# Kernel optimization log

Measured on AMD Instinct MI355X. Metric: run time of the kernel, lower is better.

Reference implementation:

```python
import jax, jax.numpy as jnp
import numpy as np

N_NODE = 4096
N_FEA_IN = 128
N_FEA_OUT = 128


def setup_inputs() -> dict:
    key = jax.random.key(0)
    k_x, k_a, k_w, k_att = jax.random.split(key, 4)
    stdv_w = 1.0 / np.sqrt(N_FEA_OUT)       # torch reset: 1/sqrt(W.size(1))
    stdv_a = 1.0 / np.sqrt(2 * N_FEA_OUT)   # a is [1, 2*n_fea_out]
    X = jax.random.normal(k_x, (N_NODE, N_FEA_IN), dtype=jnp.float32)
    A = jax.random.uniform(k_a, (N_NODE, N_NODE), dtype=jnp.float32)  # dense weighted adjacency
    W = jax.random.uniform(k_w, (N_FEA_IN, N_FEA_OUT), minval=-stdv_w, maxval=stdv_w, dtype=jnp.float32)
    a = jax.random.uniform(k_att, (1, 2 * N_FEA_OUT), minval=-stdv_a, maxval=stdv_a, dtype=jnp.float32)
    return {"X": X, "A": A, "W": W, "a": a}


def reference(X, A, W, a):
    # XW: [N, F_out]
    XW = jnp.matmul(X, W)
    f = W.shape[1]
    # Z[i,j] = concat(XW[j], XW[i]); Z @ a.T decomposes into two rank-1 broadcasts:
    s_col = jnp.matmul(XW, a[0, :f])   # depends on column index j
    s_row = jnp.matmul(XW, a[0, f:])   # depends on row index i
    Z1 = jax.nn.leaky_relu(s_row[:, None] + s_col[None, :], negative_slope=0.01)  # [N, N]
    den = jnp.exp(Z1)                  # [N, N]
    num = jnp.matmul(A, den)           # numerator[i,j] = sum_k A[i,k] * den[k,j]
    # vectorized replacement of the Python double loop: att = den/num where num != 0
    att = jnp.where(num != 0, den / jnp.where(num != 0, num, 1.0), 0.0)
    H = jnp.matmul(A, jnp.matmul(att, XW))
    return H
```

## Files before the change

kernel.cpp:

```cpp
#include <hip/hip_runtime.h>
#include <hip/hip_bf16.h>
#include <stdint.h>

#define NN 4096
#define NF 128
#define NSPLIT 16
#define XROWS 4

using f32x4  = __attribute__((ext_vector_type(4))) float;
using bf16x8 = __attribute__((ext_vector_type(8))) __bf16;
using u16x8  = __attribute__((ext_vector_type(8))) uint16_t;

__device__ __forceinline__ uint16_t f2b(float f) {
    union { float f; uint32_t u; } v; v.f = f;
    uint32_t r = v.u + 0x7FFFu + ((v.u >> 16) & 1u);
    return (uint16_t)(r >> 16);
}

__device__ __forceinline__ float b2f(uint16_t u) {
    union { uint32_t u; float f; } v; v.u = ((uint32_t)u) << 16;
    return v.f;
}

__global__ __launch_bounds__(128) void xw_kernel(
    const float* __restrict__ X, const float* __restrict__ W,
    const float* __restrict__ a,
    uint16_t* __restrict__ XWT,
    float* __restrict__ s_col, float* __restrict__ s_row) {
    __shared__ float xs[XROWS][NF];
    __shared__ float red[XROWS][2][2];
    const int i0 = blockIdx.x * XROWS, f = threadIdx.x;
    #pragma unroll
    for (int r = 0; r < XROWS; ++r) xs[r][f] = X[(size_t)(i0 + r) * NF + f];
    __syncthreads();
    float acc[XROWS] = {0.f, 0.f, 0.f, 0.f};
    #pragma unroll 4
    for (int k = 0; k < NF; ++k) {
        const float w = W[k * NF + f];
        #pragma unroll
        for (int r = 0; r < XROWS; ++r) acc[r] += xs[r][k] * w;
    }
    ushort4 xo;
    xo.x = f2b(acc[0]); xo.y = f2b(acc[1]); xo.z = f2b(acc[2]); xo.w = f2b(acc[3]);
    *(ushort4*)(XWT + (size_t)f * NN + i0) = xo;
    const float a1 = a[f], a2 = a[NF + f];
    #pragma unroll
    for (int r = 0; r < XROWS; ++r) {
        float sc = acc[r] * a1;
        float sr = acc[r] * a2;
        #pragma unroll
        for (int off = 32; off; off >>= 1) {
            sc += __shfl_down(sc, off);
            sr += __shfl_down(sr, off);
        }
        if ((f & 63) == 0) { red[r][f >> 6][0] = sc; red[r][f >> 6][1] = sr; }
    }
    __syncthreads();
    if (f < XROWS) {
        s_col[i0 + f] = red[f][0][0] + red[f][1][0];
        s_row[i0 + f] = red[f][0][1] + red[f][1][1];
    }
}

__global__ __launch_bounds__(256) void prep_kernel(
    const float* __restrict__ s_row, const float* __restrict__ s_col,
    int* __restrict__ ks, float* __restrict__ w1s, float* __restrict__ w2s,
    float4* __restrict__ rec) {
    __shared__ __align__(16) float sr[NN];
    const int t = threadIdx.x;
    #pragma unroll
    for (int c = 0; c < 16; ++c) sr[t + c * 256] = s_row[t + c * 256];
    __syncthreads();
    const bool isC = blockIdx.x >= 128;
    const int tgt = (blockIdx.x & 127) * 32 + (t >> 3);
    const int sub = t & 7;
    const float4* sr4 = (const float4*)sr;
    int cnt = 0;
    if (!isC) {
        const float s = sr[tgt];
        #pragma unroll 4
        for (int q = 0; q < 128; ++q) {
            const int k4 = q * 8 + sub;
            float4 v = sr4[k4];
            const int kb = k4 * 4;
            cnt += (v.x < s) | ((v.x == s) & (kb + 0 < tgt));
            cnt += (v.y < s) | ((v.y == s) & (kb + 1 < tgt));
            cnt += (v.z < s) | ((v.z == s) & (kb + 2 < tgt));
            cnt += (v.w < s) | ((v.w == s) & (kb + 3 < tgt));
        }
    } else {
        const float th = -s_col[tgt];
        #pragma unroll 4
        for (int q = 0; q < 128; ++q) {
            float4 v = sr4[q * 8 + sub];
            cnt += (v.x <= th) + (v.y <= th) + (v.z <= th) + (v.w <= th);
        }
    }
    cnt += __shfl_down(cnt, 4);
    cnt += __shfl_down(cnt, 2);
    cnt += __shfl_down(cnt, 1);
    if (sub == 0) {
        if (!isC) {
            const float s = sr[tgt];
            ks[cnt]  = tgt;
            w1s[cnt] = __expf(s);
            w2s[cnt] = __expf(0.01f * s);
        } else {
            const float sc = s_col[tgt];
            rec[tgt] = (float4){__int_as_float(cnt), __expf(sc), __expf(0.01f * sc), sc};
        }
    }
}

#define PB(b) ((b) + (((b) >> 4) << 1))

__global__ __launch_bounds__(512, 8) void row_kernel(
    const float* __restrict__ A,
    const float* __restrict__ s_row,
    const int* __restrict__ ks, const float* __restrict__ w1s, const float* __restrict__ w2s,
    const float4* __restrict__ rec,
    uint16_t* __restrict__ Ab, uint16_t* __restrict__ att) {
    __shared__ __align__(16) float rowA[NN];
    __shared__ __align__(16) uint16_t S1[4640];
    __shared__ __align__(16) uint16_t S2[4640];
    __shared__ float wtot[2][8];
    const int i = blockIdx.x, t = threadIdx.x;

    {
        const float4* Ar = (const float4*)(A + (size_t)i * NN);
        ushort4* Abr = (ushort4*)(Ab + (size_t)i * NN);
        #pragma unroll
        for (int c = 0; c < 2; ++c) {
            float4 v = Ar[t + c * 512];
            ((float4*)rowA)[t + c * 512] = v;
            ushort4 o; o.x = f2b(v.x); o.y = f2b(v.y); o.z = f2b(v.z); o.w = f2b(v.w);
            Abr[t + c * 512] = o;
        }
    }
    __syncthreads();

    float l1[8], l2[8];
    {
        const int4*   k4 = (const int4*)ks;
        const float4* a4 = (const float4*)w1s;
        const float4* b4 = (const float4*)w2s;
        float run1 = 0.f, run2 = 0.f;
        #pragma unroll
        for (int g = 0; g < 2; ++g) {
            int4   kk = k4[2 * t + g];
            float4 wa = a4[2 * t + g];
            float4 wb = b4[2 * t + g];
            float g0 = rowA[kk.x], g1 = rowA[kk.y], g2 = rowA[kk.z], g3 = rowA[kk.w];
            run1 += g0 * wa.x; l1[4 * g + 0] = run1;  run2 += g0 * wb.x; l2[4 * g + 0] = run2;
            run1 += g1 * wa.y; l1[4 * g + 1] = run1;  run2 += g1 * wb.y; l2[4 * g + 1] = run2;
            run1 += g2 * wa.z; l1[4 * g + 2] = run1;  run2 += g2 * wb.z; l2[4 * g + 2] = run2;
            run1 += g3 * wa.w; l1[4 * g + 3] = run1;  run2 += g3 * wb.w; l2[4 * g + 3] = run2;
        }
    }
    float s1 = l1[7], s2 = l2[7];
    const int lane = t & 63, wid = t >> 6;
    #pragma unroll
    for (int off = 1; off < 64; off <<= 1) {
        float u1 = __shfl_up(s1, off);
        float u2 = __shfl_up(s2, off);
        if (lane >= off) { s1 += u1; s2 += u2; }
    }
    if (lane == 63) { wtot[0][wid] = s1; wtot[1][wid] = s2; }
    __syncthreads();

    float off1 = 0.f, off2 = 0.f, tot1 = 0.f, tot2 = 0.f;
    #pragma unroll
    for (int w = 0; w < 8; ++w) {
        const float va = wtot[0][w], vb = wtot[1][w];
        tot1 += va; tot2 += vb;
        if (w < wid) { off1 += va; off2 += vb; }
    }
    const float ex1 = off1 + s1 - l1[7];
    const float ex2 = off2 + s2 - l2[7];
    {
        uint32_t* q1 = (uint32_t*)S1;
        uint32_t* q2 = (uint32_t*)S2;
        const int qb = t * 4 + (t >> 1);
        #pragma unroll
        for (int m = 0; m < 4; ++m) {
            const float pl1 = m ? l1[2 * m - 1] : 0.f;
            const float pl2 = m ? l2[2 * m - 1] : 0.f;
            const float sa = tot1 - ex1 - pl1;
            const float sb = tot1 - ex1 - l1[2 * m];
            const float pa = ex2 + pl2;
            const float pb = ex2 + l2[2 * m];
            q1[qb + m] = (uint32_t)f2b(sa) | ((uint32_t)f2b(sb) << 16);
            q2[qb + m] = (uint32_t)f2b(pa) | ((uint32_t)f2b(pb) << 16);
        }
    }
    if (t == 511) {
        S1[PB(4096)] = 0;
        S2[PB(4096)] = f2b(tot2);
    }
    __syncthreads();

    const float sri = s_row[i];
    uint32_t* attR = (uint32_t*)(att + (size_t)i * NN);
    #pragma unroll
    for (int e = 0; e < 4; ++e) {
        const int j0 = e * 1024 + 2 * t;
        const float4 ra = rec[j0];
        const float4 rb = rec[j0 + 1];
        const int Ca = __float_as_int(ra.x);
        const int Cb = __float_as_int(rb.x);
        const float numa = ra.y * b2f(S1[PB(Ca)]) + ra.z * b2f(S2[PB(Ca)]);
        const float numb = rb.y * b2f(S1[PB(Cb)]) + rb.z * b2f(S2[PB(Cb)]);
        float za = sri + ra.w; za = za > 0.f ? za : 0.01f * za;
        float zb = sri + rb.w; zb = zb > 0.f ? zb : 0.01f * zb;
        const float dena = __expf(za);
        const float denb = __expf(zb);
        const float va = (numa != 0.f) ? dena * __builtin_amdgcn_rcpf(numa) : 0.f;
        const float vb = (numb != 0.f) ? denb * __builtin_amdgcn_rcpf(numb) : 0.f;
        attR[e * 512 + t] = (uint32_t)f2b(va) | ((uint32_t)f2b(vb) << 16);
    }
}

__global__ __launch_bounds__(256) void gemm_splitk_kernel(
    const uint16_t* __restrict__ Abt, const uint16_t* __restrict__ Bt,
    float* __restrict__ P) {
    const int bm0 = blockIdx.y * 128;
    const int split = blockIdx.z;
    const int kBeg = split * (NN / NSPLIT);
    const int lane = threadIdx.x & 63, wid = threadIdx.x >> 6;
    const int wy = wid >> 1, wx = wid & 1;
    const int quad = lane >> 4, l16 = lane & 15;

    f32x4 acc[4][4];
    #pragma unroll
    for (int mi = 0; mi < 4; ++mi)
        #pragma unroll
        for (int ni = 0; ni < 4; ++ni)
            acc[mi][ni] = (f32x4){0.f, 0.f, 0.f, 0.f};

    const uint16_t* Ap = Abt + (size_t)(bm0 + wy * 64 + l16) * NN + quad * 8;
    const uint16_t* Bp = Bt  + (size_t)(wx * 64 + l16) * NN + quad * 8;

    #pragma unroll 2
    for (int kk = 0; kk < NN / NSPLIT; kk += 32) {
        const int k0 = kBeg + kk;
        bf16x8 af[4], bf[4];
        #pragma unroll
        for (int mi = 0; mi < 4; ++mi)
            af[mi] = *(const bf16x8*)(Ap + (size_t)(mi * 16) * NN + k0);
        #pragma unroll
        for (int ni = 0; ni < 4; ++ni)
            bf[ni] = *(const bf16x8*)(Bp + (size_t)(ni * 16) * NN + k0);
        #pragma unroll
        for (int mi = 0; mi < 4; ++mi)
            #pragma unroll
            for (int ni = 0; ni < 4; ++ni)
                acc[mi][ni] = __builtin_amdgcn_mfma_f32_16x16x32_bf16(af[mi], bf[ni], acc[mi][ni], 0, 0, 0);
    }

    float* Pp = P + (size_t)split * (NN * NF);
    #pragma unroll
    for (int mi = 0; mi < 4; ++mi) {
        const int i0 = bm0 + wy * 64 + mi * 16 + quad * 4;
        #pragma unroll
        for (int ni = 0; ni < 4; ++ni) {
            const int j = wx * 64 + ni * 16 + l16;
            *(f32x4*)(Pp + (size_t)j * NN + i0) = acc[mi][ni];
        }
    }
}

__global__ __launch_bounds__(256) void reduce_t_kernel(
    const float* __restrict__ P, uint16_t* __restrict__ M1T) {
    const int idx = (blockIdx.x * 256 + threadIdx.x) * 4;
    f32x4 s = (f32x4){0.f, 0.f, 0.f, 0.f};
    #pragma unroll
    for (int sp = 0; sp < NSPLIT; ++sp)
        s += *(const f32x4*)(P + (size_t)sp * (NN * NF) + idx);
    ushort4 o;
    o.x = f2b(s[0]); o.y = f2b(s[1]); o.z = f2b(s[2]); o.w = f2b(s[3]);
    *(ushort4*)(M1T + idx) = o;
}

__global__ __launch_bounds__(256) void reduce_out_kernel(
    const float* __restrict__ P, float* __restrict__ out) {
    __shared__ float acc[NF][17];
    const int i0 = blockIdx.x * 16;
    const int t = threadIdx.x;
    const int ii = t & 15, jb = t >> 4;
    float local[8];
    #pragma unroll
    for (int jj = 0; jj < 8; ++jj) local[jj] = 0.f;
    for (int sp = 0; sp < NSPLIT; ++sp) {
        const float* Pp = P + (size_t)sp * (NN * NF) + i0 + ii;
        #pragma unroll
        for (int jj = 0; jj < 8; ++jj)
            local[jj] += Pp[(size_t)(jb + jj * 16) * NN];
    }
    #pragma unroll
    for (int jj = 0; jj < 8; ++jj) acc[jb + jj * 16][ii] = local[jj];
    __syncthreads();
    const int j = t & 127, rb = t >> 7;
    #pragma unroll
    for (int p = 0; p < 8; ++p) {
        const int r = rb + p * 2;
        out[(size_t)(i0 + r) * NF + j] = acc[j][r];
    }
}

extern "C" void kernel_launch(void* const* d_in, const int* in_sizes, int n_in,
                              void* d_out, int out_size, void* d_ws, size_t ws_size,
                              hipStream_t stream) {
    (void)in_sizes; (void)n_in; (void)out_size; (void)ws_size;
    const float* X = (const float*)d_in[0];
    const float* A = (const float*)d_in[1];
    const float* W = (const float*)d_in[2];
    const float* a = (const float*)d_in[3];
    float* H = (float*)d_out;

    char* ws = (char*)d_ws;
    uint16_t* Ab  = (uint16_t*)(ws);
    uint16_t* att = (uint16_t*)(ws + ((size_t)32 << 20));
    float*    P   = (float*)   (ws + ((size_t)64 << 20));
    uint16_t* XWT = (uint16_t*)(ws + ((size_t)96 << 20));
    uint16_t* M1T = (uint16_t*)(ws + ((size_t)97 << 20));
    char* sm = ws + ((size_t)64 << 20);
    float*  s_col = (float*) (sm);
    float*  s_row = (float*) (sm + (16 << 10));
    int*    ks    = (int*)   (sm + (32 << 10));
    float*  w1s   = (float*) (sm + (48 << 10));
    float*  w2s   = (float*) (sm + (64 << 10));
    float4* rec   = (float4*)(sm + (80 << 10));

    xw_kernel<<<NN / XROWS, NF, 0, stream>>>(X, W, a, XWT, s_col, s_row);
    prep_kernel<<<256, 256, 0, stream>>>(s_row, s_col, ks, w1s, w2s, rec);
    row_kernel<<<NN, 512, 0, stream>>>(A, s_row, ks, w1s, w2s, rec, Ab, att);
    gemm_splitk_kernel<<<dim3(1, 32, NSPLIT), 256, 0, stream>>>(att, XWT, P);
    reduce_t_kernel<<<(NN * NF / 4) / 256, 256, 0, stream>>>(P, M1T);
    gemm_splitk_kernel<<<dim3(1, 32, NSPLIT), 256, 0, stream>>>(Ab, M1T, P);
    reduce_out_kernel<<<NN / 16, 256, 0, stream>>>(P, H);
}
```

Measured before the change: 209.9 us.

## Halve GEMM block tile and software-pipeline split-K register loads

```diff
diff --git a/kernel.cpp b/kernel.cpp
--- a/kernel.cpp
+++ b/kernel.cpp
@@ -220,47 +220,60 @@
     }
 }
 
+#define GLOAD(af, bf, kq)                                                     \
+    {                                                                         \
+        af[0] = *(const bf16x8*)(Ap + (size_t)0  * NN + (kq));                \
+        af[1] = *(const bf16x8*)(Ap + (size_t)16 * NN + (kq));                \
+        bf[0] = *(const bf16x8*)(Bp + (size_t)0  * NN + (kq));                \
+        bf[1] = *(const bf16x8*)(Bp + (size_t)16 * NN + (kq));                \
+        bf[2] = *(const bf16x8*)(Bp + (size_t)32 * NN + (kq));                \
+        bf[3] = *(const bf16x8*)(Bp + (size_t)48 * NN + (kq));                \
+    }
+
+#define MFMA_SET(af, bf)                                                      \
+    {                                                                         \
+        _Pragma("unroll")                                                     \
+        for (int mi = 0; mi < 2; ++mi)                                        \
+            _Pragma("unroll")                                                 \
+            for (int ni = 0; ni < 4; ++ni)                                    \
+                acc[mi][ni] = __builtin_amdgcn_mfma_f32_16x16x32_bf16(        \
+                    af[mi], bf[ni], acc[mi][ni], 0, 0, 0);                    \
+    }
+
 __global__ __launch_bounds__(256) void gemm_splitk_kernel(
     const uint16_t* __restrict__ Abt, const uint16_t* __restrict__ Bt,
     float* __restrict__ P) {
-    const int bm0 = blockIdx.y * 128;
+    const int bm0 = blockIdx.y * 64;
     const int split = blockIdx.z;
     const int kBeg = split * (NN / NSPLIT);
     const int lane = threadIdx.x & 63, wid = threadIdx.x >> 6;
     const int wy = wid >> 1, wx = wid & 1;
     const int quad = lane >> 4, l16 = lane & 15;
 
-    f32x4 acc[4][4];
-    #pragma unroll
-    for (int mi = 0; mi < 4; ++mi)
+    f32x4 acc[2][4];
+    #pragma unroll
+    for (int mi = 0; mi < 2; ++mi)
         #pragma unroll
         for (int ni = 0; ni < 4; ++ni)
             acc[mi][ni] = (f32x4){0.f, 0.f, 0.f, 0.f};
 
-    const uint16_t* Ap = Abt + (size_t)(bm0 + wy * 64 + l16) * NN + quad * 8;
+    const uint16_t* Ap = Abt + (size_t)(bm0 + wy * 32 + l16) * NN + quad * 8;
     const uint16_t* Bp = Bt  + (size_t)(wx * 64 + l16) * NN + quad * 8;
 
-    #pragma unroll 2
-    for (int kk = 0; kk < NN / NSPLIT; kk += 32) {
-        const int k0 = kBeg + kk;
-        bf16x8 af[4], bf[4];
-        #pragma unroll
-        for (int mi = 0; mi < 4; ++mi)
-            af[mi] = *(const bf16x8*)(Ap + (size_t)(mi * 16) * NN + k0);
-        #pragma unroll
-        for (int ni = 0; ni < 4; ++ni)
-            bf[ni] = *(const bf16x8*)(Bp + (size_t)(ni * 16) * NN + k0);
-        #pragma unroll
-        for (int mi = 0; mi < 4; ++mi)
-            #pragma unroll
-            for (int ni = 0; ni < 4; ++ni)
-                acc[mi][ni] = __builtin_amdgcn_mfma_f32_16x16x32_bf16(af[mi], bf[ni], acc[mi][ni], 0, 0, 0);
+    bf16x8 a0[2], b0[4], a1[2], b1[4];
+    GLOAD(a0, b0, kBeg);
+    #pragma unroll
+    for (int kk = 0; kk < NN / NSPLIT; kk += 64) {
+        GLOAD(a1, b1, kBeg + kk + 32);
+        MFMA_SET(a0, b0);
+        if (kk + 64 < NN / NSPLIT) GLOAD(a0, b0, kBeg + kk + 64);
+        MFMA_SET(a1, b1);
     }
 
     float* Pp = P + (size_t)split * (NN * NF);
     #pragma unroll
-    for (int mi = 0; mi < 4; ++mi) {
-        const int i0 = bm0 + wy * 64 + mi * 16 + quad * 4;
+    for (int mi = 0; mi < 2; ++mi) {
+        const int i0 = bm0 + wy * 32 + mi * 16 + quad * 4;
         #pragma unroll
         for (int ni = 0; ni < 4; ++ni) {
             const int j = wx * 64 + ni * 16 + l16;
@@ -334,8 +347,8 @@
     xw_kernel<<<NN / XROWS, NF, 0, stream>>>(X, W, a, XWT, s_col, s_row);
     prep_kernel<<<256, 256, 0, stream>>>(s_row, s_col, ks, w1s, w2s, rec);
     row_kernel<<<NN, 512, 0, stream>>>(A, s_row, ks, w1s, w2s, rec, Ab, att);
-    gemm_splitk_kernel<<<dim3(1, 32, NSPLIT), 256, 0, stream>>>(att, XWT, P);
+    gemm_splitk_kernel<<<dim3(1, 64, NSPLIT), 256, 0, stream>>>(att, XWT, P);
     reduce_t_kernel<<<(NN * NF / 4) / 256, 256, 0, stream>>>(P, M1T);
-    gemm_splitk_kernel<<<dim3(1, 32, NSPLIT), 256, 0, stream>>>(Ab, M1T, P);
+    gemm_splitk_kernel<<<dim3(1, 64, NSPLIT), 256, 0, stream>>>(Ab, M1T, P);
     reduce_out_kernel<<<NN / 16, 256, 0, stream>>>(P, H);
 }
```

New measurement: 220.2 us. 4.9% more time.

## Replace split-K GEMMs and reduce kernels with in-block split-K LDS reduction

Applied to the files above, without the earlier changes.

```diff
diff --git a/kernel.cpp b/kernel.cpp
--- a/kernel.cpp
+++ b/kernel.cpp
@@ -4,7 +4,6 @@
 
 #define NN 4096
 #define NF 128
-#define NSPLIT 16
 #define XROWS 4
 
 using f32x4  = __attribute__((ext_vector_type(4))) float;
@@ -220,90 +219,91 @@
     }
 }
 
-__global__ __launch_bounds__(256) void gemm_splitk_kernel(
-    const uint16_t* __restrict__ Abt, const uint16_t* __restrict__ Bt,
-    float* __restrict__ P) {
-    const int bm0 = blockIdx.y * 128;
-    const int split = blockIdx.z;
-    const int kBeg = split * (NN / NSPLIT);
-    const int lane = threadIdx.x & 63, wid = threadIdx.x >> 6;
-    const int wy = wid >> 1, wx = wid & 1;
-    const int quad = lane >> 4, l16 = lane & 15;
-
-    f32x4 acc[4][4];
-    #pragma unroll
-    for (int mi = 0; mi < 4; ++mi)
-        #pragma unroll
-        for (int ni = 0; ni < 4; ++ni)
-            acc[mi][ni] = (f32x4){0.f, 0.f, 0.f, 0.f};
-
-    const uint16_t* Ap = Abt + (size_t)(bm0 + wy * 64 + l16) * NN + quad * 8;
-    const uint16_t* Bp = Bt  + (size_t)(wx * 64 + l16) * NN + quad * 8;
-
-    #pragma unroll 2
-    for (int kk = 0; kk < NN / NSPLIT; kk += 32) {
+__device__ __forceinline__ void gemm16_core(
+    const uint16_t* __restrict__ Aop, const uint16_t* __restrict__ Bop,
+    int i0, float* __restrict__ red, float2* __restrict__ v) {
+    const int t = threadIdx.x;
+    const int lane = t & 63, wv = t >> 6;
+    const int l16 = lane & 15, quad = lane >> 4;
+    const int kBeg = wv * 256;
+
+    f32x4 acc[8];
+    #pragma unroll
+    for (int ni = 0; ni < 8; ++ni) acc[ni] = (f32x4){0.f, 0.f, 0.f, 0.f};
+
+    const uint16_t* Ap = Aop + (size_t)(i0 + l16) * NN + quad * 8;
+    const uint16_t* Bp = Bop + (size_t)l16 * NN + quad * 8;
+
+    #pragma unroll
+    for (int kk = 0; kk < 256; kk += 32) {
         const int k0 = kBeg + kk;
-        bf16x8 af[4], bf[4];
-        #pragma unroll
-        for (int mi = 0; mi < 4; ++mi)
-            af[mi] = *(const bf16x8*)(Ap + (size_t)(mi * 16) * NN + k0);
-        #pragma unroll
-        for (int ni = 0; ni < 4; ++ni)
-            bf[ni] = *(const bf16x8*)(Bp + (size_t)(ni * 16) * NN + k0);
-        #pragma unroll
-        for (int mi = 0; mi < 4; ++mi)
-            #pragma unroll
-            for (int ni = 0; ni < 4; ++ni)
-                acc[mi][ni] = __builtin_amdgcn_mfma_f32_16x16x32_bf16(af[mi], bf[ni], acc[mi][ni], 0, 0, 0);
-    }
-
-    float* Pp = P + (size_t)split * (NN * NF);
-    #pragma unroll
-    for (int mi = 0; mi < 4; ++mi) {
-        const int i0 = bm0 + wy * 64 + mi * 16 + quad * 4;
-        #pragma unroll
-        for (int ni = 0; ni < 4; ++ni) {
-            const int j = wx * 64 + ni * 16 + l16;
-            *(f32x4*)(Pp + (size_t)j * NN + i0) = acc[mi][ni];
-        }
-    }
-}
-
-__global__ __launch_bounds__(256) void reduce_t_kernel(
-    const float* __restrict__ P, uint16_t* __restrict__ M1T) {
-    const int idx = (blockIdx.x * 256 + threadIdx.x) * 4;
-    f32x4 s = (f32x4){0.f, 0.f, 0.f, 0.f};
-    #pragma unroll
-    for (int sp = 0; sp < NSPLIT; ++sp)
-        s += *(const f32x4*)(P + (size_t)sp * (NN * NF) + idx);
-    ushort4 o;
-    o.x = f2b(s[0]); o.y = f2b(s[1]); o.z = f2b(s[2]); o.w = f2b(s[3]);
-    *(ushort4*)(M1T + idx) = o;
-}
-
-__global__ __launch_bounds__(256) void reduce_out_kernel(
-    const float* __restrict__ P, float* __restrict__ out) {
-    __shared__ float acc[NF][17];
+        const bf16x8 af = *(const bf16x8*)(Ap + k0);
+        #pragma unroll
+        for (int ni = 0; ni < 8; ++ni) {
+            const bf16x8 bf = *(const bf16x8*)(Bp + (size_t)(ni * 16) * NN + k0);
+            acc[ni] = __builtin_amdgcn_mfma_f32_16x16x32_bf16(af, bf, acc[ni], 0, 0, 0);
+        }
+    }
+
+    float* img = red + (wv & 3) * 2048;
+    const int base = l16 * 16 + quad * 4;
+    #pragma unroll
+    for (int ph = 0; ph < 4; ++ph) {
+        if ((wv >> 2) == ph) {
+            if (ph == 0) {
+                #pragma unroll
+                for (int ni = 0; ni < 8; ++ni)
+                    *(f32x4*)(img + ni * 256 + base) = acc[ni];
+            } else {
+                #pragma unroll
+                for (int ni = 0; ni < 8; ++ni) {
+                    f32x4 x = *(const f32x4*)(img + ni * 256 + base);
+                    *(f32x4*)(img + ni * 256 + base) = x + acc[ni];
+                }
+            }
+        }
+        __syncthreads();
+    }
+    float2 s = {0.f, 0.f};
+    #pragma unroll
+    for (int im = 0; im < 4; ++im) {
+        const float2 x = *(const float2*)(red + im * 2048 + 2 * t);
+        s.x += x.x; s.y += x.y;
+    }
+    *v = s;
+}
+
+__global__ __launch_bounds__(1024, 4) void gemm_fused_m1(
+    const uint16_t* __restrict__ Aop, const uint16_t* __restrict__ Bop,
+    uint16_t* __restrict__ M1T) {
+    __shared__ __align__(16) float red[4 * 2048];
     const int i0 = blockIdx.x * 16;
+    float2 v;
+    gemm16_core(Aop, Bop, i0, red, &v);
+    const int p = 2 * threadIdx.x;
+    const int f = p >> 4, il = p & 15;
+    ushort2 o; o.x = f2b(v.x); o.y = f2b(v.y);
+    *(ushort2*)(M1T + (size_t)f * NN + i0 + il) = o;
+}
+
+__global__ __launch_bounds__(1024, 4) void gemm_fused_h(
+    const uint16_t* __restrict__ Aop, const uint16_t* __restrict__ Bop,
+    float* __restrict__ H) {
+    __shared__ __align__(16) float red[4 * 2048];
+    __shared__ __align__(16) float lds2[16][132];
+    const int i0 = blockIdx.x * 16;
+    float2 v;
+    gemm16_core(Aop, Bop, i0, red, &v);
+    const int p = 2 * threadIdx.x;
+    const int f = p >> 4, il = p & 15;
+    lds2[il][f] = v.x;
+    lds2[il + 1][f] = v.y;
+    __syncthreads();
     const int t = threadIdx.x;
-    const int ii = t & 15, jb = t >> 4;
-    float local[8];
-    #pragma unroll
-    for (int jj = 0; jj < 8; ++jj) local[jj] = 0.f;
-    for (int sp = 0; sp < NSPLIT; ++sp) {
-        const float* Pp = P + (size_t)sp * (NN * NF) + i0 + ii;
-        #pragma unroll
-        for (int jj = 0; jj < 8; ++jj)
-            local[jj] += Pp[(size_t)(jb + jj * 16) * NN];
-    }
-    #pragma unroll
-    for (int jj = 0; jj < 8; ++jj) acc[jb + jj * 16][ii] = local[jj];
-    __syncthreads();
-    const int j = t & 127, rb = t >> 7;
-    #pragma unroll
-    for (int p = 0; p < 8; ++p) {
-        const int r = rb + p * 2;
-        out[(size_t)(i0 + r) * NF + j] = acc[j][r];
+    if (t < 512) {
+        const int r = t >> 5, fq = t & 31;
+        const float4 x = *(const float4*)(&lds2[r][fq * 4]);
+        *(float4*)(H + (size_t)(i0 + r) * NF + fq * 4) = x;
     }
 }
 
@@ -320,7 +320,6 @@
     char* ws = (char*)d_ws;
     uint16_t* Ab  = (uint16_t*)(ws);
     uint16_t* att = (uint16_t*)(ws + ((size_t)32 << 20));
-    float*    P   = (float*)   (ws + ((size_t)64 << 20));
     uint16_t* XWT = (uint16_t*)(ws + ((size_t)96 << 20));
     uint16_t* M1T = (uint16_t*)(ws + ((size_t)97 << 20));
     char* sm = ws + ((size_t)64 << 20);
@@ -334,8 +333,6 @@
     xw_kernel<<<NN / XROWS, NF, 0, stream>>>(X, W, a, XWT, s_col, s_row);
     prep_kernel<<<256, 256, 0, stream>>>(s_row, s_col, ks, w1s, w2s, rec);
     row_kernel<<<NN, 512, 0, stream>>>(A, s_row, ks, w1s, w2s, rec, Ab, att);
-    gemm_splitk_kernel<<<dim3(1, 32, NSPLIT), 256, 0, stream>>>(att, XWT, P);
-    reduce_t_kernel<<<(NN * NF / 4) / 256, 256, 0, stream>>>(P, M1T);
-    gemm_splitk_kernel<<<dim3(1, 32, NSPLIT), 256, 0, stream>>>(Ab, M1T, P);
-    reduce_out_kernel<<<NN / 16, 256, 0, stream>>>(P, H);
-}
+    gemm_fused_m1<<<NN / 16, 1024, 0, stream>>>(att, XWT, M1T);
+    gemm_fused_h<<<NN / 16, 1024, 0, stream>>>(Ab, M1T, H);
+}
```

After: 217.4 us. +3.6%, slower.
